# Kernel optimization log

Hardware: AMD Instinct MI355X
Metric: run time of the kernel (lower is better)

## Reference

```python
import jax, jax.numpy as jnp
import numpy as np

NUM_HEADS = 12

def setup_inputs() -> dict:
    key = jax.random.key(0)
    ks = jax.random.split(key, 6)
    B, N, C, T = 1, 4096, 768, 16
    return {
        "x": jax.random.normal(ks[0], (B, N, C), dtype=jnp.float32),
        "templates": jax.random.normal(ks[1], (T, 3 * C, C), dtype=jnp.float32) * 0.02,
        "coeffs": jax.random.normal(ks[2], (2, T, 1), dtype=jnp.float32),
        "qkv_bias": jnp.zeros((3 * C,), dtype=jnp.float32),
        "proj_w": jax.random.normal(ks[3], (C, C), dtype=jnp.float32) * 0.02,
        "proj_b": jnp.zeros((C,), dtype=jnp.float32),
    }

def reference(x, templates, coeffs, qkv_bias, proj_w, proj_b):
    B, N, C = x.shape
    H = NUM_HEADS
    hd = C // H
    scale = hd ** -0.5
    # template bank: each of num_cf coefficient sets builds a (3C, C) weight; average them
    num_cf = coeffs.shape[0]
    qkv_w = jnp.einsum('kt,toi->oi', coeffs[:, :, 0], templates) / num_cf  # (3C, C)
    qkv = x @ qkv_w.T + qkv_bias                                          # (B, N, 3C)
    qkv = qkv.reshape(B, N, 3, H, hd).transpose(2, 0, 3, 1, 4)            # (3, B, H, N, hd)
    q, k, v = qkv[0], qkv[1], qkv[2]
    attn = jax.nn.softmax(jnp.einsum('bhnd,bhmd->bhnm', q, k) * scale, axis=-1)
    out = jnp.einsum('bhnm,bhmd->bhnd', attn, v)                          # (B, H, N, hd)
    out = out.transpose(0, 2, 1, 3).reshape(B, N, C)
    return out @ proj_w.T + proj_b
```

## Files before the change

kernel.cpp:

```cpp
#include <hip/hip_runtime.h>
#include <stdint.h>

#define N_SEQ 4096
#define C_DIM 768
#define HEADS 12
#define HD    64
#define OI    (2304*768)

typedef __attribute__((ext_vector_type(8))) short short8;
typedef __attribute__((ext_vector_type(4))) float f32x4;
typedef __attribute__((ext_vector_type(16))) float f32x16;

__device__ __forceinline__ short f2bf(float f) {
  union { float f; unsigned u; } v; v.f = f;
  unsigned r = v.u + 0x7FFF + ((v.u >> 16) & 1);
  return (short)(r >> 16);
}
__device__ __forceinline__ short f2bf_trunc(float f) {
  union { float f; unsigned u; } v; v.f = f;
  return (short)(v.u >> 16);
}

__global__ __launch_bounds__(256) void prep_qkvw(const float* __restrict__ tmpl,
                                                 const float* __restrict__ coeffs,
                                                 short* __restrict__ w_bf) {
  __shared__ float c[16];
  if (threadIdx.x < 16)
    c[threadIdx.x] = 0.5f * (coeffs[threadIdx.x] + coeffs[16 + threadIdx.x]);
  __syncthreads();
  int idx = blockIdx.x * 256 + threadIdx.x;
  int base = idx * 4;
  if (base >= OI) return;
  float ax = 0.f, ay = 0.f, az = 0.f, aw = 0.f;
#pragma unroll
  for (int t = 0; t < 16; ++t) {
    float4 v = *(const float4*)(tmpl + (size_t)t * OI + base);
    float ct = c[t];
    ax = fmaf(ct, v.x, ax); ay = fmaf(ct, v.y, ay);
    az = fmaf(ct, v.z, az); aw = fmaf(ct, v.w, aw);
  }
  short4 o = make_short4(f2bf(ax), f2bf(ay), f2bf(az), f2bf(aw));
  *(short4*)(w_bf + base) = o;
}

__global__ __launch_bounds__(256) void cvt_bf16(const float* __restrict__ src,
                                                short* __restrict__ dst, int n4) {
  int i = blockIdx.x * 256 + threadIdx.x;
  if (i >= n4) return;
  float4 v = ((const float4*)src)[i];
  ((short4*)dst)[i] = make_short4(f2bf(v.x), f2bf(v.y), f2bf(v.z), f2bf(v.w));
}

#define GST 40
#define QSCALE 0.1803368801111204f
__global__ __launch_bounds__(256) void gemm_qkv(const short* __restrict__ A,
                                                const short* __restrict__ B,
                                                const float* __restrict__ bias,
                                                short* __restrict__ qkv_out) {
  __shared__ short As[128 * GST];
  __shared__ short Bs[128 * GST];
  int tid = threadIdx.x;
  int wave = tid >> 6, lane = tid & 63, g = lane >> 4, l15 = lane & 15;
  int wm = (wave >> 1) * 64, wn = (wave & 1) * 64;
  size_t mblk = (size_t)blockIdx.x * 128;
  size_t nblk = (size_t)blockIdx.y * 128;

  f32x4 acc[4][4];
#pragma unroll
  for (int mi = 0; mi < 4; ++mi)
#pragma unroll
    for (int ni = 0; ni < 4; ++ni)
#pragma unroll
      for (int r = 0; r < 4; ++r) acc[mi][ni][r] = 0.f;

  int row0 = tid >> 2;
  int c8   = (tid & 3) * 8;

  for (int k0 = 0; k0 < 768; k0 += 32) {
    short8 a0 = *(const short8*)(A + (mblk + row0) * 768 + k0 + c8);
    short8 a1 = *(const short8*)(A + (mblk + row0 + 64) * 768 + k0 + c8);
    short8 b0 = *(const short8*)(B + (nblk + row0) * 768 + k0 + c8);
    short8 b1 = *(const short8*)(B + (nblk + row0 + 64) * 768 + k0 + c8);
    __syncthreads();
    *(short8*)(As + row0 * GST + c8) = a0;
    *(short8*)(As + (row0 + 64) * GST + c8) = a1;
    *(short8*)(Bs + row0 * GST + c8) = b0;
    *(short8*)(Bs + (row0 + 64) * GST + c8) = b1;
    __syncthreads();
    short8 af[4], bfr[4];
#pragma unroll
    for (int mi = 0; mi < 4; ++mi)
      af[mi] = *(const short8*)(As + (wm + mi * 16 + l15) * GST + g * 8);
#pragma unroll
    for (int ni = 0; ni < 4; ++ni)
      bfr[ni] = *(const short8*)(Bs + (wn + ni * 16 + l15) * GST + g * 8);
#pragma unroll
    for (int mi = 0; mi < 4; ++mi)
#pragma unroll
      for (int ni = 0; ni < 4; ++ni)
        acc[mi][ni] = __builtin_amdgcn_mfma_f32_16x16x32_bf16(af[mi], bfr[ni], acc[mi][ni], 0, 0, 0);
  }

#pragma unroll
  for (int ni = 0; ni < 4; ++ni) {
    int col = (int)nblk + wn + ni * 16 + l15;
    int which = col / 768;
    int rem = col - which * 768;
    int h = rem >> 6, d = rem & 63;
    float bcol = bias[col];
    if (which == 2) {
      short* vbase = qkv_out + (size_t)2 * HEADS * N_SEQ * HD
                   + ((size_t)h * HD + d) * N_SEQ;
#pragma unroll
      for (int mi = 0; mi < 4; ++mi) {
        int rowb = (int)mblk + wm + mi * 16 + g * 4;
        short4 o;
        o.x = f2bf(acc[mi][ni][0] + bcol);
        o.y = f2bf(acc[mi][ni][1] + bcol);
        o.z = f2bf(acc[mi][ni][2] + bcol);
        o.w = f2bf(acc[mi][ni][3] + bcol);
        *(short4*)(vbase + rowb) = o;
      }
    } else {
      float sc = (which == 0) ? QSCALE : 1.0f;
      short* dst = qkv_out + ((size_t)which * HEADS + h) * N_SEQ * HD + d;
#pragma unroll
      for (int mi = 0; mi < 4; ++mi) {
        int rowb = (int)mblk + wm + mi * 16 + g * 4;
#pragma unroll
        for (int r = 0; r < 4; ++r)
          dst[(size_t)(rowb + r) * HD] = f2bf((acc[mi][ni][r] + bcol) * sc);
      }
    }
  }
}

__global__ __launch_bounds__(256) void gemm_proj(const short* __restrict__ A,
                                                 const short* __restrict__ B,
                                                 const float* __restrict__ bias,
                                                 float* __restrict__ C) {
  __shared__ short As[64 * GST];
  __shared__ short Bs[64 * GST];
  int tid = threadIdx.x;
  int wave = tid >> 6, lane = tid & 63, g = lane >> 4, l15 = lane & 15;
  int wm = (wave >> 1) * 32, wn = (wave & 1) * 32;
  size_t mblk = (size_t)blockIdx.x * 64;
  size_t nblk = (size_t)blockIdx.y * 64;

  f32x4 acc[2][2];
#pragma unroll
  for (int mi = 0; mi < 2; ++mi)
#pragma unroll
    for (int ni = 0; ni < 2; ++ni)
#pragma unroll
      for (int r = 0; r < 4; ++r) acc[mi][ni][r] = 0.f;

  int row0 = tid >> 2;
  int c8   = (tid & 3) * 8;

  for (int k0 = 0; k0 < 768; k0 += 32) {
    short8 a0 = *(const short8*)(A + (mblk + row0) * 768 + k0 + c8);
    short8 b0 = *(const short8*)(B + (nblk + row0) * 768 + k0 + c8);
    __syncthreads();
    *(short8*)(As + row0 * GST + c8) = a0;
    *(short8*)(Bs + row0 * GST + c8) = b0;
    __syncthreads();
    short8 af[2], bfr[2];
#pragma unroll
    for (int mi = 0; mi < 2; ++mi)
      af[mi] = *(const short8*)(As + (wm + mi * 16 + l15) * GST + g * 8);
#pragma unroll
    for (int ni = 0; ni < 2; ++ni)
      bfr[ni] = *(const short8*)(Bs + (wn + ni * 16 + l15) * GST + g * 8);
#pragma unroll
    for (int mi = 0; mi < 2; ++mi)
#pragma unroll
      for (int ni = 0; ni < 2; ++ni)
        acc[mi][ni] = __builtin_amdgcn_mfma_f32_16x16x32_bf16(af[mi], bfr[ni], acc[mi][ni], 0, 0, 0);
  }

#pragma unroll
  for (int ni = 0; ni < 2; ++ni) {
    int col = (int)nblk + wn + ni * 16 + l15;
    float bcol = bias[col];
#pragma unroll
    for (int mi = 0; mi < 2; ++mi) {
      int rowb = (int)mblk + wm + mi * 16 + g * 4;
#pragma unroll
      for (int r = 0; r < 4; ++r)
        C[(size_t)(rowb + r) * 768 + col] = acc[mi][ni][r] + bcol;
    }
  }
}

#define PST 68
__global__ __launch_bounds__(128, 2) void attn_fa(const short* __restrict__ qkv_buf,
                                                  float* __restrict__ op0,
                                                  float* __restrict__ op1,
                                                  float* __restrict__ lp) {
  __shared__ short Ks[64 * PST];
  __shared__ short Vt[64 * PST];
  __shared__ short Ps[128 * PST];
  int bid = blockIdx.x;
  int j = (bid & 7) * 96 + (bid >> 3);
  int h = j >> 6;
  int rj = j & 63;
  int half = rj >> 5;
  int qt = rj & 31;
  int tid = threadIdx.x, wave = tid >> 6, lane = tid & 63;
  int q5 = lane & 31, h5 = lane >> 5;
  int qb = qt * 128 + wave * 64;
  int kvb = half * 2048;
  const short* qh  = qkv_buf + (size_t)(0 * HEADS + h) * N_SEQ * HD;
  const short* kh  = qkv_buf + (size_t)(1 * HEADS + h) * N_SEQ * HD;
  const short* vth = qkv_buf + (size_t)2 * HEADS * N_SEQ * HD + (size_t)h * HD * N_SEQ;

  short8 qf[2][4];
#pragma unroll
  for (int s = 0; s < 2; ++s)
#pragma unroll
    for (int c = 0; c < 4; ++c)
      qf[s][c] = *(const short8*)(qh + (size_t)(qb + s * 32 + q5) * HD + c * 16 + h5 * 8);

  f32x16 o_acc[2][2];
#pragma unroll
  for (int s = 0; s < 2; ++s)
#pragma unroll
    for (int dt = 0; dt < 2; ++dt)
#pragma unroll
      for (int r = 0; r < 16; ++r) o_acc[s][dt][r] = 0.f;
  float l_r[2] = {0.f, 0.f};

  int srow = tid >> 1;
  int shalf = (tid & 1) * 32;

  short8 kr[4], vr[4];
#pragma unroll
  for (int i = 0; i < 4; ++i) {
    kr[i] = *(const short8*)(kh + (size_t)(kvb + srow) * HD + shalf + 8 * i);
    vr[i] = *(const short8*)(vth + (size_t)srow * N_SEQ + kvb + shalf + 8 * i);
  }

  short* pw = Ps + wave * 64 * PST;

  for (int t0 = kvb; t0 < kvb + 2048; t0 += 64) {
    __syncthreads();
#pragma unroll
    for (int i = 0; i < 4; ++i) {
      *(short8*)(Ks + srow * PST + shalf + 8 * i) = kr[i];
      *(short8*)(Vt + srow * PST + shalf + 8 * i) = vr[i];
    }
    __syncthreads();

    if (t0 + 64 < kvb + 2048) {
      int t1 = t0 + 64;
#pragma unroll
      for (int i = 0; i < 4; ++i) {
        kr[i] = *(const short8*)(kh + (size_t)(t1 + srow) * HD + shalf + 8 * i);
        vr[i] = *(const short8*)(vth + (size_t)srow * N_SEQ + t1 + shalf + 8 * i);
      }
    }

    f32x16 st[2][2];
#pragma unroll
    for (int s = 0; s < 2; ++s)
#pragma unroll
      for (int kt = 0; kt < 2; ++kt)
#pragma unroll
        for (int r = 0; r < 16; ++r) st[s][kt][r] = 0.f;
#pragma unroll
    for (int c = 0; c < 4; ++c)
#pragma unroll
      for (int kt = 0; kt < 2; ++kt) {
        short8 kf = *(const short8*)(Ks + (kt * 32 + q5) * PST + c * 16 + h5 * 8);
#pragma unroll
        for (int s = 0; s < 2; ++s)
          st[s][kt] = __builtin_amdgcn_mfma_f32_32x32x16_bf16(kf, qf[s][c], st[s][kt], 0, 0, 0);
      }

#pragma unroll
    for (int s = 0; s < 2; ++s)
#pragma unroll
      for (int kt = 0; kt < 2; ++kt)
#pragma unroll
        for (int cc = 0; cc < 4; ++cc) {
          float p0 = __builtin_amdgcn_exp2f(st[s][kt][cc * 4 + 0]);
          float p1 = __builtin_amdgcn_exp2f(st[s][kt][cc * 4 + 1]);
          float p2 = __builtin_amdgcn_exp2f(st[s][kt][cc * 4 + 2]);
          float p3 = __builtin_amdgcn_exp2f(st[s][kt][cc * 4 + 3]);
          l_r[s] += (p0 + p1) + (p2 + p3);
          short4 o = make_short4(f2bf_trunc(p0), f2bf_trunc(p1), f2bf_trunc(p2), f2bf_trunc(p3));
          *(short4*)(pw + (s * 32 + q5) * PST + kt * 32 + cc * 8 + h5 * 4) = o;
        }

#pragma unroll
    for (int c = 0; c < 4; ++c) {
      short8 pf[2];
#pragma unroll
      for (int s = 0; s < 2; ++s)
        pf[s] = *(const short8*)(pw + (s * 32 + q5) * PST + c * 16 + h5 * 8);
#pragma unroll
      for (int dt = 0; dt < 2; ++dt) {
        short8 vf = *(const short8*)(Vt + (dt * 32 + q5) * PST + c * 16 + h5 * 8);
#pragma unroll
        for (int s = 0; s < 2; ++s)
          o_acc[s][dt] = __builtin_amdgcn_mfma_f32_32x32x16_bf16(pf[s], vf, o_acc[s][dt], 0, 0, 0);
      }
    }
  }

  float* op = half ? op1 : op0;
#pragma unroll
  for (int s = 0; s < 2; ++s) {
    float l = l_r[s] + __shfl_xor(l_r[s], 32);
#pragma unroll
    for (int cc = 0; cc < 4; ++cc)
#pragma unroll
      for (int rr = 0; rr < 4; ++rr) {
        int qloc = rr + 8 * cc + 4 * h5;
        size_t base = ((size_t)h * N_SEQ + qb + s * 32 + qloc) * HD;
#pragma unroll
        for (int dt = 0; dt < 2; ++dt)
          op[base + dt * 32 + q5] = o_acc[s][dt][cc * 4 + rr];
      }
    if (h5 == 0)
      lp[((size_t)half * HEADS + h) * N_SEQ + qb + s * 32 + q5] = l;
  }
}

__global__ __launch_bounds__(256) void attn_reduce(const float* __restrict__ op0,
                                                   const float* __restrict__ op1,
                                                   const float* __restrict__ lp,
                                                   short* __restrict__ out_bf) {
  int idx = blockIdx.x * 256 + threadIdx.x;
  int d4 = idx & 15;
  int n  = (idx >> 4) & 4095;
  int h  = idx >> 16;
  size_t o = ((size_t)h * N_SEQ + n) * HD + d4 * 4;
  float4 a = *(const float4*)(op0 + o);
  float4 b = *(const float4*)(op1 + o);
  float l = lp[(size_t)h * N_SEQ + n] + lp[((size_t)HEADS + h) * N_SEQ + n];
  float inv = 1.0f / l;
  short4 s = make_short4(f2bf((a.x + b.x) * inv), f2bf((a.y + b.y) * inv),
                         f2bf((a.z + b.z) * inv), f2bf((a.w + b.w) * inv));
  *(short4*)(out_bf + (size_t)n * C_DIM + h * HD + d4 * 4) = s;
}

extern "C" void kernel_launch(void* const* d_in, const int* in_sizes, int n_in,
                              void* d_out, int out_size, void* d_ws, size_t ws_size,
                              hipStream_t stream) {
  const float* x        = (const float*)d_in[0];
  const float* tmpl     = (const float*)d_in[1];
  const float* coeffs   = (const float*)d_in[2];
  const float* qkv_bias = (const float*)d_in[3];
  const float* proj_w   = (const float*)d_in[4];
  const float* proj_b   = (const float*)d_in[5];
  float* out = (float*)d_out;
  char* ws = (char*)d_ws;

  short* w_bf    = (short*)(ws);
  short* x_bf    = (short*)(ws + 3538944);
  short* pw_bf   = (short*)(ws + 9830400);
  short* qkvb    = (short*)(ws + 11010048);
  short* attn_bf = (short*)(ws + 29884416);
  float* opart1  = (float*)(ws + 36175872);
  float* lpart   = (float*)(ws + 48758784);
  float* opart0  = out;

  prep_qkvw<<<1728, 256, 0, stream>>>(tmpl, coeffs, w_bf);
  cvt_bf16<<<3072, 256, 0, stream>>>(x, x_bf, 786432);
  cvt_bf16<<<576, 256, 0, stream>>>(proj_w, pw_bf, 147456);

  dim3 g1(32, 18);
  gemm_qkv<<<g1, 256, 0, stream>>>(x_bf, w_bf, qkv_bias, qkvb);

  attn_fa<<<768, 128, 0, stream>>>(qkvb, opart0, opart1, lpart);
  attn_reduce<<<3072, 256, 0, stream>>>(opart0, opart1, lpart, attn_bf);

  dim3 g2(64, 12);
  gemm_proj<<<g2, 256, 0, stream>>>(attn_bf, pw_bf, proj_b, out);
}
```

Baseline: 334.3 us.

## Split attention block across four waves with 32 query rows each

The flash-attention kernel now runs 256 threads (four waves) per block instead of two. Each wave handles 32 query rows instead of 64, and K/V staging into shared memory is spread over four threads per row. This halves per-wave register state (accumulators, Q fragments) to raise occupancy and latency hiding. In exchange, each K/V fragment read from shared memory now feeds half as many MFMAs, so LDS traffic rises relative to math.

Measured after the change: 339.6 us. About the same (+1.6%).

```diff
diff --git a/kernel.cpp b/kernel.cpp
--- a/kernel.cpp
+++ b/kernel.cpp
@@ -194,7 +194,7 @@
 }
 
 #define PST 68
-__global__ __launch_bounds__(128, 2) void attn_fa(const short* __restrict__ qkv_buf,
+__global__ __launch_bounds__(256, 2) void attn_fa(const short* __restrict__ qkv_buf,
                                                   float* __restrict__ op0,
                                                   float* __restrict__ op1,
                                                   float* __restrict__ lp) {
@@ -209,123 +209,105 @@
   int qt = rj & 31;
   int tid = threadIdx.x, wave = tid >> 6, lane = tid & 63;
   int q5 = lane & 31, h5 = lane >> 5;
-  int qb = qt * 128 + wave * 64;
+  int qb = qt * 128 + wave * 32;
   int kvb = half * 2048;
   const short* qh  = qkv_buf + (size_t)(0 * HEADS + h) * N_SEQ * HD;
   const short* kh  = qkv_buf + (size_t)(1 * HEADS + h) * N_SEQ * HD;
   const short* vth = qkv_buf + (size_t)2 * HEADS * N_SEQ * HD + (size_t)h * HD * N_SEQ;
 
-  short8 qf[2][4];
-#pragma unroll
-  for (int s = 0; s < 2; ++s)
-#pragma unroll
-    for (int c = 0; c < 4; ++c)
-      qf[s][c] = *(const short8*)(qh + (size_t)(qb + s * 32 + q5) * HD + c * 16 + h5 * 8);
-
-  f32x16 o_acc[2][2];
-#pragma unroll
-  for (int s = 0; s < 2; ++s)
-#pragma unroll
-    for (int dt = 0; dt < 2; ++dt)
-#pragma unroll
-      for (int r = 0; r < 16; ++r) o_acc[s][dt][r] = 0.f;
-  float l_r[2] = {0.f, 0.f};
-
-  int srow = tid >> 1;
-  int shalf = (tid & 1) * 32;
-
-  short8 kr[4], vr[4];
-#pragma unroll
-  for (int i = 0; i < 4; ++i) {
-    kr[i] = *(const short8*)(kh + (size_t)(kvb + srow) * HD + shalf + 8 * i);
-    vr[i] = *(const short8*)(vth + (size_t)srow * N_SEQ + kvb + shalf + 8 * i);
-  }
-
-  short* pw = Ps + wave * 64 * PST;
+  short8 qf[4];
+#pragma unroll
+  for (int c = 0; c < 4; ++c)
+    qf[c] = *(const short8*)(qh + (size_t)(qb + q5) * HD + c * 16 + h5 * 8);
+
+  f32x16 o_acc[2];
+#pragma unroll
+  for (int dt = 0; dt < 2; ++dt)
+#pragma unroll
+    for (int r = 0; r < 16; ++r) o_acc[dt][r] = 0.f;
+  float l_r = 0.f;
+
+  int srow = tid >> 2;
+  int sq   = (tid & 3) * 16;
+
+  short8 kr[2], vr[2];
+#pragma unroll
+  for (int i = 0; i < 2; ++i) {
+    kr[i] = *(const short8*)(kh + (size_t)(kvb + srow) * HD + sq + 8 * i);
+    vr[i] = *(const short8*)(vth + (size_t)srow * N_SEQ + kvb + sq + 8 * i);
+  }
+
+  short* pw = Ps + wave * 32 * PST;
 
   for (int t0 = kvb; t0 < kvb + 2048; t0 += 64) {
     __syncthreads();
 #pragma unroll
-    for (int i = 0; i < 4; ++i) {
-      *(short8*)(Ks + srow * PST + shalf + 8 * i) = kr[i];
-      *(short8*)(Vt + srow * PST + shalf + 8 * i) = vr[i];
+    for (int i = 0; i < 2; ++i) {
+      *(short8*)(Ks + srow * PST + sq + 8 * i) = kr[i];
+      *(short8*)(Vt + srow * PST + sq + 8 * i) = vr[i];
     }
     __syncthreads();
 
     if (t0 + 64 < kvb + 2048) {
       int t1 = t0 + 64;
 #pragma unroll
-      for (int i = 0; i < 4; ++i) {
-        kr[i] = *(const short8*)(kh + (size_t)(t1 + srow) * HD + shalf + 8 * i);
-        vr[i] = *(const short8*)(vth + (size_t)srow * N_SEQ + t1 + shalf + 8 * i);
-      }
-    }
-
-    f32x16 st[2][2];
-#pragma unroll
-    for (int s = 0; s < 2; ++s)
-#pragma unroll
-      for (int kt = 0; kt < 2; ++kt)
-#pragma unroll
-        for (int r = 0; r < 16; ++r) st[s][kt][r] = 0.f;
+      for (int i = 0; i < 2; ++i) {
+        kr[i] = *(const short8*)(kh + (size_t)(t1 + srow) * HD + sq + 8 * i);
+        vr[i] = *(const short8*)(vth + (size_t)srow * N_SEQ + t1 + sq + 8 * i);
+      }
+    }
+
+    f32x16 st[2];
+#pragma unroll
+    for (int kt = 0; kt < 2; ++kt)
+#pragma unroll
+      for (int r = 0; r < 16; ++r) st[kt][r] = 0.f;
 #pragma unroll
     for (int c = 0; c < 4; ++c)
 #pragma unroll
       for (int kt = 0; kt < 2; ++kt) {
         short8 kf = *(const short8*)(Ks + (kt * 32 + q5) * PST + c * 16 + h5 * 8);
-#pragma unroll
-        for (int s = 0; s < 2; ++s)
-          st[s][kt] = __builtin_amdgcn_mfma_f32_32x32x16_bf16(kf, qf[s][c], st[s][kt], 0, 0, 0);
-      }
-
-#pragma unroll
-    for (int s = 0; s < 2; ++s)
-#pragma unroll
-      for (int kt = 0; kt < 2; ++kt)
-#pragma unroll
-        for (int cc = 0; cc < 4; ++cc) {
-          float p0 = __builtin_amdgcn_exp2f(st[s][kt][cc * 4 + 0]);
-          float p1 = __builtin_amdgcn_exp2f(st[s][kt][cc * 4 + 1]);
-          float p2 = __builtin_amdgcn_exp2f(st[s][kt][cc * 4 + 2]);
-          float p3 = __builtin_amdgcn_exp2f(st[s][kt][cc * 4 + 3]);
-          l_r[s] += (p0 + p1) + (p2 + p3);
-          short4 o = make_short4(f2bf_trunc(p0), f2bf_trunc(p1), f2bf_trunc(p2), f2bf_trunc(p3));
-          *(short4*)(pw + (s * 32 + q5) * PST + kt * 32 + cc * 8 + h5 * 4) = o;
-        }
+        st[kt] = __builtin_amdgcn_mfma_f32_32x32x16_bf16(kf, qf[c], st[kt], 0, 0, 0);
+      }
+
+#pragma unroll
+    for (int kt = 0; kt < 2; ++kt)
+#pragma unroll
+      for (int cc = 0; cc < 4; ++cc) {
+        float p0 = __builtin_amdgcn_exp2f(st[kt][cc * 4 + 0]);
+        float p1 = __builtin_amdgcn_exp2f(st[kt][cc * 4 + 1]);
+        float p2 = __builtin_amdgcn_exp2f(st[kt][cc * 4 + 2]);
+        float p3 = __builtin_amdgcn_exp2f(st[kt][cc * 4 + 3]);
+        l_r += (p0 + p1) + (p2 + p3);
+        short4 o = make_short4(f2bf_trunc(p0), f2bf_trunc(p1), f2bf_trunc(p2), f2bf_trunc(p3));
+        *(short4*)(pw + q5 * PST + kt * 32 + cc * 8 + h5 * 4) = o;
+      }
 
 #pragma unroll
     for (int c = 0; c < 4; ++c) {
-      short8 pf[2];
-#pragma unroll
-      for (int s = 0; s < 2; ++s)
-        pf[s] = *(const short8*)(pw + (s * 32 + q5) * PST + c * 16 + h5 * 8);
+      short8 pf = *(const short8*)(pw + q5 * PST + c * 16 + h5 * 8);
 #pragma unroll
       for (int dt = 0; dt < 2; ++dt) {
         short8 vf = *(const short8*)(Vt + (dt * 32 + q5) * PST + c * 16 + h5 * 8);
-#pragma unroll
-        for (int s = 0; s < 2; ++s)
-          o_acc[s][dt] = __builtin_amdgcn_mfma_f32_32x32x16_bf16(pf[s], vf, o_acc[s][dt], 0, 0, 0);
+        o_acc[dt] = __builtin_amdgcn_mfma_f32_32x32x16_bf16(pf, vf, o_acc[dt], 0, 0, 0);
       }
     }
   }
 
   float* op = half ? op1 : op0;
-#pragma unroll
-  for (int s = 0; s < 2; ++s) {
-    float l = l_r[s] + __shfl_xor(l_r[s], 32);
-#pragma unroll
-    for (int cc = 0; cc < 4; ++cc)
-#pragma unroll
-      for (int rr = 0; rr < 4; ++rr) {
-        int qloc = rr + 8 * cc + 4 * h5;
-        size_t base = ((size_t)h * N_SEQ + qb + s * 32 + qloc) * HD;
-#pragma unroll
-        for (int dt = 0; dt < 2; ++dt)
-          op[base + dt * 32 + q5] = o_acc[s][dt][cc * 4 + rr];
-      }
-    if (h5 == 0)
-      lp[((size_t)half * HEADS + h) * N_SEQ + qb + s * 32 + q5] = l;
-  }
+  float l = l_r + __shfl_xor(l_r, 32);
+#pragma unroll
+  for (int cc = 0; cc < 4; ++cc)
+#pragma unroll
+    for (int rr = 0; rr < 4; ++rr) {
+      int qloc = rr + 8 * cc + 4 * h5;
+      size_t base = ((size_t)h * N_SEQ + qb + qloc) * HD;
+#pragma unroll
+      for (int dt = 0; dt < 2; ++dt)
+        op[base + dt * 32 + q5] = o_acc[dt][cc * 4 + rr];
+    }
+  if (h5 == 0)
+    lp[((size_t)half * HEADS + h) * N_SEQ + qb + q5] = l;
 }
 
 __global__ __launch_bounds__(256) void attn_reduce(const float* __restrict__ op0,
@@ -374,7 +356,7 @@
   dim3 g1(32, 18);
   gemm_qkv<<<g1, 256, 0, stream>>>(x_bf, w_bf, qkv_bias, qkvb);
 
-  attn_fa<<<768, 128, 0, stream>>>(qkvb, opart0, opart1, lpart);
+  attn_fa<<<768, 256, 0, stream>>>(qkvb, opart0, opart1, lpart);
   attn_reduce<<<3072, 256, 0, stream>>>(opart0, opart1, lpart, attn_bf);
 
   dim3 g2(64, 12);
```
